# Kernel tuning notes

Hardware: AMD Instinct MI355X
Metric: run time of the kernel (lower is better)

## Reference

```python
import jax, jax.numpy as jnp
import numpy as np
from functools import partial

DN = ('NCHW', 'OIHW', 'NCHW')

def conv2d(x, w, b, stride):
    y = jax.lax.conv_general_dilated(x, w, (stride, stride), 'VALID', dimension_numbers=DN)
    return y + b[None, :, None, None]

def squash(s, eps=1e-8):
    norm = jnp.linalg.norm(s, axis=-1, keepdims=True)
    return (norm ** 2 / (1 + norm ** 2)) * s / (norm + eps)

def setup_inputs() -> dict:
    key = jax.random.key(0)
    ks = jax.random.split(key, 10)
    B, H, W = 16, 32, 512
    F, CAPS, E, OD = 64, 8, 8, 16
    H1 = (H - 6) // 2 + 1          # 14
    W1 = (W - 6) // 2 + 1          # 254
    N = F * H1 * W1 // CAPS        # 28448
    s = 0.05
    return {
        'x': jax.random.normal(ks[0], (B, H, W), jnp.float32),
        'conv1_w': jax.random.normal(ks[1], (F, 1, 6, 6), jnp.float32) * s,
        'conv1_b': jnp.zeros((F,), jnp.float32),
        'conv2_w': jax.random.normal(ks[2], (F, F, 6, 6), jnp.float32) * s,
        'conv2_b': jnp.zeros((F,), jnp.float32),
        'conv3_w': jax.random.normal(ks[3], (F, 2 * F, 1, 1), jnp.float32) * s,
        'conv3_b': jnp.zeros((F,), jnp.float32),
        'pc_w': jax.random.normal(ks[4], (N, CAPS, CAPS), jnp.float32) * s,  # [N, in, out]
        'pc_b': jnp.zeros((N, CAPS), jnp.float32),
        'ec_w': jax.random.normal(ks[5], (N, E, OD, CAPS), jnp.float32),
    }

def reference(x, conv1_w, conv1_b, conv2_w, conv2_b, conv3_w, conv3_b, pc_w, pc_b, ec_w):
    CAPS = pc_w.shape[1]
    NUM_ITER = 3
    B = x.shape[0]
    h = x[:, None]                                  # [B,1,H,W]
    h = jax.nn.relu(conv2d(h, conv1_w, conv1_b, 2)) # [B,F,14,254]
    y = jnp.pad(h, ((0, 0), (0, 0), (2, 3), (2, 3)))  # ZeroPad2d((2,3,2,3))
    y = jax.nn.relu(conv2d(y, conv2_w, conv2_b, 1))
    h = jax.nn.relu(jnp.concatenate((h, y), axis=1))
    h = conv2d(h, conv3_w, conv3_b, 1)              # [B,F,14,254]
    u_in = h.reshape(B, -1, CAPS)                   # [B,N,caps_len]
    # PrimaryCaps: N independent Linear(caps,caps) -> one batched einsum
    u = jnp.einsum('bni,nio->bno', u_in, pc_w) + pc_b[None]
    # EmotionCaps: per-capsule prediction u_hat [B,N,E,out_dim]
    u_hat = jnp.einsum('neoi,bni->bneo', ec_w, u)
    N, E = ec_w.shape[0], ec_w.shape[1]
    b_log = jnp.zeros((B, N, E), u_hat.dtype)
    v = None
    for r in range(NUM_ITER):
        c = jax.nn.softmax(b_log, axis=2)           # [B,N,E]
        s = jnp.einsum('bne,bneo->beo', c, u_hat)   # [B,E,out_dim]
        v = squash(s)
        if r < NUM_ITER - 1:
            b_log = b_log + jnp.einsum('bneo,beo->bne', u_hat, v)
    return jnp.linalg.norm(v, axis=-1)              # [B,E]
```

## Files before the change

kernel.cpp:

```cpp
#include <hip/hip_runtime.h>
#include <hip/hip_bf16.h>
#include <math.h>

#define BB 16
#define H1 14
#define W1 254
#define HPH 19
#define HPW2 264
#define NCAP 28448
#define FLATSZ 227584

typedef __attribute__((ext_vector_type(8))) short bf16x8;
typedef __attribute__((ext_vector_type(4))) float f32x4;
typedef __attribute__((ext_vector_type(2))) __fp16 f16x2;
typedef __attribute__((ext_vector_type(4))) uint uint4v;

__device__ __forceinline__ ushort f2bf(float f) {
  __hip_bfloat16 h = __float2bfloat16(f);
  return *(ushort*)&h;
}

__global__ __launch_bounds__(256) void prep_w(const float* __restrict__ w2, const float* __restrict__ w3,
                                              ushort* __restrict__ wb, float* __restrict__ w3t) {
  int idx = blockIdx.x * 256 + threadIdx.x;
  if (idx < 147456) {
    int co = idx / 2304; int rem = idx - co * 2304;
    int tap = rem >> 6; int ci = rem & 63;
    wb[idx] = f2bf(w2[(co * 64 + ci) * 36 + tap]);
  }
  if (idx < 8192) {
    int co = idx & 63; int c = idx >> 6;
    w3t[idx] = w3[co * 128 + c];
  }
}

__global__ __launch_bounds__(256) void cvt_ec(const float* __restrict__ ecw, uint* __restrict__ ech) {
  size_t i = (size_t)blockIdx.x * 256 + threadIdx.x;
  const float4* s = (const float4*)ecw + i * 2;
  float4 a = s[0], b = s[1];
  uint4v pk;
  { f16x2 h = __builtin_amdgcn_cvt_pkrtz(a.x, a.y); pk.x = *(uint*)&h; }
  { f16x2 h = __builtin_amdgcn_cvt_pkrtz(a.z, a.w); pk.y = *(uint*)&h; }
  { f16x2 h = __builtin_amdgcn_cvt_pkrtz(b.x, b.y); pk.z = *(uint*)&h; }
  { f16x2 h = __builtin_amdgcn_cvt_pkrtz(b.z, b.w); pk.w = *(uint*)&h; }
  *((uint4v*)ech + i) = pk;
}

__global__ __launch_bounds__(256) void conv1_k(const float* __restrict__ x, const float* __restrict__ w1,
                                               const float* __restrict__ b1, float* __restrict__ hc) {
  const int i = blockIdx.x, b = blockIdx.y;
  __shared__ float xs[6 * 512];
  __shared__ float wsh[2304];
  __shared__ float bsh[64];
  const int t = threadIdx.x;
  for (int idx = t; idx < 6 * 512; idx += 256) {
    int r = idx >> 9, c = idx & 511;
    xs[idx] = x[((size_t)b * 32 + 2 * i + r) * 512 + c];
  }
  for (int idx = t; idx < 2304; idx += 256) wsh[idx] = w1[idx];
  if (t < 64) bsh[t] = b1[t];
  __syncthreads();
  if (t < 254) {
    for (int c = 0; c < 64; c++) {
      float acc = bsh[c];
#pragma unroll
      for (int p = 0; p < 6; p++)
#pragma unroll
        for (int q = 0; q < 6; q++)
          acc = fmaf(xs[p * 512 + 2 * t + q], wsh[c * 36 + p * 6 + q], acc);
      acc = fmaxf(acc, 0.f);
      hc[(((size_t)b * 64 + c) * H1 + i) * W1 + t] = acc;
    }
  }
}

__global__ __launch_bounds__(256) void nhwc_k(const float* __restrict__ hc, ushort* __restrict__ hpc) {
  const int ct = blockIdx.x, i = blockIdx.y, b = blockIdx.z;
  const int c0 = ct * 64;
  __shared__ float ls[64 * 65];
  const int t = threadIdx.x;
  for (int idx = t; idx < 4096; idx += 256) {
    int ci = idx >> 6, cc = idx & 63;
    int c = c0 + cc;
    ls[ci * 65 + cc] = (c < W1) ? hc[(((size_t)b * 64 + ci) * H1 + i) * W1 + c] : 0.f;
  }
  __syncthreads();
  uint* outp = (uint*)hpc;
  for (int idx = t; idx < 2048; idx += 256) {
    int cc = idx >> 5, ci2 = idx & 31;
    int c = c0 + cc;
    if (c < W1) {
      float f0 = ls[(2 * ci2) * 65 + cc];
      float f1 = ls[(2 * ci2 + 1) * 65 + cc];
      uint pk = (uint)f2bf(f0) | ((uint)f2bf(f1) << 16);
      outp[(((size_t)b * HPH + 2 + i) * HPW2 + 2 + c) * 32 + ci2] = pk;
    }
  }
}

__device__ __forceinline__ void stage_b(const ushort* __restrict__ wb, ushort* __restrict__ bbuf,
                                        int tap, int w, int l) {
#pragma unroll
  for (int r = 0; r < 2; r++) {
    int v = r * 256 + w * 64 + l;
    int co = v >> 3, s = v & 7;
    int g = s ^ (co & 7);
    const ushort* gp = wb + co * 2304 + tap * 64 + g * 8;
    ushort* lp = bbuf + (size_t)(r * 256 + w * 64) * 8;
    __builtin_amdgcn_global_load_lds((const uint*)gp, (uint*)lp, 16, 0, 0);
  }
}

__global__ __launch_bounds__(256, 1) void conv2_mfma(const ushort* __restrict__ hpc,
                                                     const ushort* __restrict__ wb,
                                                     const float* __restrict__ b2, float* __restrict__ y) {
  const int b = blockIdx.z, i = blockIdx.y, j0 = blockIdx.x * 128;
  const int t = threadIdx.x;
  const int w = t >> 6, l = t & 63;
  const int lr = l & 15, quad = l >> 4;

  __shared__ ushort bls[2][4096];

  f32x4 acc[2][4];
#pragma unroll
  for (int mt = 0; mt < 2; mt++)
#pragma unroll
    for (int nt = 0; nt < 4; nt++) acc[mt][nt] = (f32x4){0.f, 0.f, 0.f, 0.f};

  const ushort* abase = hpc + (((size_t)b * HPH + i) * HPW2 + (j0 + w * 32 + lr)) * 64 + quad * 8;

  bf16x8 a0[2][2], a1[2][2];

#define ALOAD(dst, tap)                                                        \
  {                                                                            \
    const int p_ = (tap) / 6, q_ = (tap) % 6;                                  \
    const ushort* ap_ = abase + ((size_t)p_ * HPW2 + q_) * 64;                 \
    dst[0][0] = *(const bf16x8*)(ap_);                                         \
    dst[0][1] = *(const bf16x8*)(ap_ + 1024);                                  \
    dst[1][0] = *(const bf16x8*)(ap_ + 32);                                    \
    dst[1][1] = *(const bf16x8*)(ap_ + 32 + 1024);                             \
  }

#define COMPUTE(a, bp)                                                         \
  {                                                                            \
    _Pragma("unroll")                                                          \
    for (int ch = 0; ch < 2; ch++) {                                           \
      const int g2 = ch * 4 + quad;                                            \
      _Pragma("unroll")                                                        \
      for (int nt = 0; nt < 4; nt++) {                                         \
        const int co = nt * 16 + lr;                                           \
        bf16x8 bf = *(const bf16x8*)((bp) + co * 64 + ((g2 ^ (co & 7)) * 8));  \
        acc[0][nt] = __builtin_amdgcn_mfma_f32_16x16x32_bf16(a[ch][0], bf, acc[0][nt], 0, 0, 0); \
        acc[1][nt] = __builtin_amdgcn_mfma_f32_16x16x32_bf16(a[ch][1], bf, acc[1][nt], 0, 0, 0); \
      }                                                                        \
    }                                                                          \
  }

  stage_b(wb, &bls[0][0], 0, w, l);
  __syncthreads();
  ALOAD(a0, 0);

  for (int tp = 0; tp < 36; tp += 2) {
    stage_b(wb, &bls[1][0], tp + 1, w, l);
    ALOAD(a1, tp + 1);
    COMPUTE(a0, &bls[0][0]);
    __syncthreads();
    if (tp + 2 < 36) {
      stage_b(wb, &bls[0][0], tp + 2, w, l);
      ALOAD(a0, tp + 2);
    }
    COMPUTE(a1, &bls[1][0]);
    __syncthreads();
  }

#pragma unroll
  for (int nt = 0; nt < 4; nt++) {
    const int co = nt * 16 + lr;
    const float bias = b2[co];
    float* yrow = y + (((size_t)b * 64 + co) * H1 + i) * W1;
#pragma unroll
    for (int mt = 0; mt < 2; mt++) {
      const int jb = j0 + w * 32 + mt * 16 + quad * 4;
#pragma unroll
      for (int r = 0; r < 4; r++) {
        int j = jb + r;
        if (j < W1) yrow[j] = fmaxf(acc[mt][nt][r] + bias, 0.f);
      }
    }
  }
#undef ALOAD
#undef COMPUTE
}

__global__ __launch_bounds__(256) void conv3_k(const float* __restrict__ hc, const float* __restrict__ y,
                                               const float* __restrict__ w3t, const float* __restrict__ b3,
                                               float* __restrict__ out3) {
  const int b = blockIdx.z, i = blockIdx.y, j0 = blockIdx.x * 64;
  __shared__ float cs[32][64];
  __shared__ float wsh[32][64];
  const int t = threadIdx.x;
  const int cog = t >> 4, jg = t & 15;
  float acc[4][4];
#pragma unroll
  for (int a = 0; a < 4; a++)
#pragma unroll
    for (int j = 0; j < 4; j++) acc[a][j] = 0.f;

  for (int ch = 0; ch < 4; ch++) {
    __syncthreads();
    for (int idx = t; idx < 2048; idx += 256) {
      int cl = idx >> 6; int j = j0 + (idx & 63);
      int c = ch * 32 + cl;
      float v = 0.f;
      if (j < W1) {
        if (c < 64) v = hc[(((size_t)b * 64 + c) * H1 + i) * W1 + j];
        else        v = y[(((size_t)b * 64 + (c - 64)) * H1 + i) * W1 + j];
      }
      cs[cl][idx & 63] = v;
    }
    for (int idx = t; idx < 2048; idx += 256)
      wsh[idx >> 6][idx & 63] = w3t[(ch * 32 + (idx >> 6)) * 64 + (idx & 63)];
    __syncthreads();
#pragma unroll
    for (int c = 0; c < 32; c++) {
      float4 xv = *(const float4*)&cs[c][jg * 4];
      float4 wv = *(const float4*)&wsh[c][cog * 4];
#pragma unroll
      for (int jj = 0; jj < 4; jj++) {
        float xx = (&xv.x)[jj];
        acc[0][jj] = fmaf(wv.x, xx, acc[0][jj]);
        acc[1][jj] = fmaf(wv.y, xx, acc[1][jj]);
        acc[2][jj] = fmaf(wv.z, xx, acc[2][jj]);
        acc[3][jj] = fmaf(wv.w, xx, acc[3][jj]);
      }
    }
  }
#pragma unroll
  for (int a = 0; a < 4; a++) {
    int co = cog * 4 + a;
    float bias = b3[co];
#pragma unroll
    for (int jj = 0; jj < 4; jj++) {
      int j = j0 + jg * 4 + jj;
      if (j < W1) out3[(((size_t)b * 64 + co) * H1 + i) * W1 + j] = acc[a][jj] + bias;
    }
  }
}

__global__ __launch_bounds__(256) void pc_k(const float* __restrict__ out3, const float* __restrict__ pcw,
                                            const float* __restrict__ pcb, float* __restrict__ u) {
  int n = blockIdx.x * 256 + threadIdx.x;
  if (n >= NCAP) return;
  float pw[64];
  const float4* pwp = (const float4*)(pcw + (size_t)n * 64);
#pragma unroll
  for (int k = 0; k < 16; k++) {
    float4 v = pwp[k];
    pw[4 * k] = v.x; pw[4 * k + 1] = v.y; pw[4 * k + 2] = v.z; pw[4 * k + 3] = v.w;
  }
  float pb[8];
  {
    const float4* pbp = (const float4*)(pcb + (size_t)n * 8);
    float4 a = pbp[0], b = pbp[1];
    pb[0] = a.x; pb[1] = a.y; pb[2] = a.z; pb[3] = a.w;
    pb[4] = b.x; pb[5] = b.y; pb[6] = b.z; pb[7] = b.w;
  }
  for (int b = 0; b < BB; b++) {
    const float4* uip = (const float4*)(out3 + (size_t)b * FLATSZ + (size_t)n * 8);
    float4 a = uip[0], c = uip[1];
    float ui[8] = {a.x, a.y, a.z, a.w, c.x, c.y, c.z, c.w};
    float uo[8];
#pragma unroll
    for (int o = 0; o < 8; o++) uo[o] = pb[o];
#pragma unroll
    for (int i2 = 0; i2 < 8; i2++)
#pragma unroll
      for (int o = 0; o < 8; o++) uo[o] = fmaf(ui[i2], pw[i2 * 8 + o], uo[o]);
    float4* up = (float4*)(u + ((size_t)b * NCAP + n) * 8);
    up[0] = make_float4(uo[0], uo[1], uo[2], uo[3]);
    up[1] = make_float4(uo[4], uo[5], uo[6], uo[7]);
  }
}

template <int CTRL>
__device__ __forceinline__ float dpp_add(float x) {
  int y = __builtin_amdgcn_update_dpp(0, __float_as_int(x), CTRL, 0xF, 0xF, true);
  return x + __int_as_float(y);
}

template <int MODE>
__global__ __launch_bounds__(256, 4) void route5_k(const float* __restrict__ u, const uint* __restrict__ ech,
                                                   const float* __restrict__ v, float* __restrict__ sout) {
  __shared__ float red[4096];
  __shared__ float vlds[1024];
  float* us = red;

  const int t = threadIdx.x, l = t & 63, wv = t >> 6;
  const int b0 = blockIdx.y * 8;
  const int n0 = blockIdx.x * 32 + wv * 8;
  const int xaddr = (l ^ 32) << 2;

  if (MODE) {
    for (int idx = t; idx < 1024; idx += 256) vlds[idx] = v[b0 * 128 + idx];
  }
#pragma unroll
  for (int bb = 0; bb < 8; bb++)
    us[wv * 512 + bb * 64 + l] = u[((size_t)(b0 + bb) * NCAP + n0) * 8 + l];
  if (MODE) __syncthreads();

  float sacc[16];
#pragma unroll
  for (int k = 0; k < 16; k++) sacc[k] = 0.f;

  const uint4v* hbase = (const uint4v*)(ech + (size_t)n0 * 512) + (l * 2);

  auto proc = [&](int nn, uint4v w0, uint4v w1) {
    float ec[16];
#pragma unroll
    for (int k = 0; k < 4; k++) {
      uint t0 = w0[k], t1 = w1[k];
      f16x2 a = *(f16x2*)&t0;
      f16x2 b = *(f16x2*)&t1;
      ec[2 * k]     = (float)a.x; ec[2 * k + 1] = (float)a.y;
      ec[8 + 2 * k] = (float)b.x; ec[8 + 2 * k + 1] = (float)b.y;
    }
#pragma unroll
    for (int bb = 0; bb < 8; bb++) {
      const float4* up = (const float4*)&us[wv * 512 + bb * 64 + nn * 8];
      const float4 ua = up[0], ub = up[1];
      const float uv[8] = {ua.x, ua.y, ua.z, ua.w, ub.x, ub.y, ub.z, ub.w};
      float h0 = 0.f, h1 = 0.f;
#pragma unroll
      for (int k = 0; k < 8; k++) {
        h0 = fmaf(ec[k], uv[k], h0);
        h1 = fmaf(ec[8 + k], uv[k], h1);
      }
      if (MODE == 0) {
        sacc[2 * bb] += h0;
        sacc[2 * bb + 1] += h1;
      } else {
        const float2 vv = *(const float2*)&vlds[bb * 128 + 2 * l];
        float p = fmaf(h0, vv.x, h1 * vv.y);
        p = dpp_add<0xB1>(p);
        p = dpp_add<0x4E>(p);
        p = dpp_add<0x141>(p);
        const float ex = __expf(p);
        float den = dpp_add<0x140>(ex);
        den += __int_as_float(__builtin_amdgcn_ds_swizzle(__float_as_int(den), 0x401F));
        den += __int_as_float(__builtin_amdgcn_ds_bpermute(xaddr, __float_as_int(den)));
        const float cc = ex * __builtin_amdgcn_rcpf(den);
        sacc[2 * bb] = fmaf(cc, h0, sacc[2 * bb]);
        sacc[2 * bb + 1] = fmaf(cc, h1, sacc[2 * bb + 1]);
      }
    }
  };

  uint4v ca0 = hbase[0], ca1 = hbase[1];
#pragma unroll 1
  for (int nn = 0; nn < 8; nn += 2) {
    const uint4v* pb = hbase + (size_t)(nn + 1) * 128;
    uint4v cb0 = pb[0], cb1 = pb[1];
    proc(nn, ca0, ca1);
    if (nn + 2 < 8) {
      const uint4v* pa = hbase + (size_t)(nn + 2) * 128;
      ca0 = pa[0]; ca1 = pa[1];
    }
    proc(nn + 1, cb0, cb1);
  }

  __syncthreads();
#pragma unroll
  for (int k = 0; k < 16; k++) red[k * 256 + wv * 64 + l] = sacc[k];
  __syncthreads();
#pragma unroll
  for (int m = 0; m < 4; m++) {
    int slot = t + 256 * m;
    int bl = slot >> 7, eo = slot & 127;
    int k = 2 * bl + (eo & 1), l2 = eo >> 1;
    const float* r = red + k * 256 + l2;
    atomicAdd(&sout[(b0 + bl) * 128 + eo], r[0] + r[64] + r[128] + r[192]);
  }
}

__global__ void squash_k(const float* __restrict__ s, float scale, const float* __restrict__ vprev,
                         float* __restrict__ vout) {
  int t = threadIdx.x;
  const float* sp = s + t * 16;
  float sv[16]; float nn = 0.f;
#pragma unroll
  for (int o = 0; o < 16; o++) { float x = sp[o] * scale; sv[o] = x; nn = fmaf(x, x, nn); }
  float norm = sqrtf(nn);
  float f = nn / (1.f + nn) / (norm + 1e-8f);
#pragma unroll
  for (int o = 0; o < 16; o++) {
    float base = vprev ? vprev[t * 16 + o] : 0.f;
    vout[t * 16 + o] = base + f * sv[o];
  }
}

__global__ void squash_out_k(const float* __restrict__ s, float* __restrict__ out) {
  int t = threadIdx.x;
  float nn = 0.f;
#pragma unroll
  for (int o = 0; o < 16; o++) { float x = s[t * 16 + o]; nn = fmaf(x, x, nn); }
  float norm = sqrtf(nn);
  float f = nn / (1.f + nn) / (norm + 1e-8f);
  out[t] = f * norm;
}

extern "C" void kernel_launch(void* const* d_in, const int* in_sizes, int n_in,
                              void* d_out, int out_size, void* d_ws, size_t ws_size,
                              hipStream_t stream) {
  const float* x   = (const float*)d_in[0];
  const float* w1  = (const float*)d_in[1];
  const float* b1  = (const float*)d_in[2];
  const float* w2  = (const float*)d_in[3];
  const float* b2  = (const float*)d_in[4];
  const float* w3  = (const float*)d_in[5];
  const float* b3  = (const float*)d_in[6];
  const float* pcw = (const float*)d_in[7];
  const float* pcb = (const float*)d_in[8];
  const float* ecw = (const float*)d_in[9];
  float* out = (float*)d_out;

  float* ws = (float*)d_ws;
  size_t o = 0;
  float* hc   = ws + o; o += 3641344;
  float* yb   = ws + o; o += 3641344;
  float* out3 = ws + o; o += 3641344;
  ushort* hpc = (ushort*)(ws + o); o += 2568192;
  ushort* wb  = (ushort*)(ws + o); o += 73728;
  float* w3t  = ws + o; o += 8192;
  float* s0   = ws + o; o += 2048;
  float* s1   = ws + o; o += 2048;
  float* s2   = ws + o; o += 2048;
  float* v0   = ws + o; o += 2048;
  float* v1   = ws + o; o += 2048;
  uint* ech   = (uint*)(ws + o); o += 14565376;
  float* ub   = hc;

  hipMemsetAsync(hpc, 0, (size_t)16 * HPH * HPW2 * 64 * 2, stream);
  hipMemsetAsync(s0, 0, 3 * 2048 * 4, stream);

  prep_w<<<576, 256, 0, stream>>>(w2, w3, wb, w3t);
  cvt_ec<<<14224, 256, 0, stream>>>(ecw, ech);
  conv1_k<<<dim3(14, 16), 256, 0, stream>>>(x, w1, b1, hc);
  nhwc_k<<<dim3(4, 14, 16), 256, 0, stream>>>(hc, hpc);
  conv2_mfma<<<dim3(2, 14, 16), 256, 0, stream>>>(hpc, wb, b2, yb);
  conv3_k<<<dim3(4, 14, 16), 256, 0, stream>>>(hc, yb, w3t, b3, out3);
  pc_k<<<112, 256, 0, stream>>>(out3, pcw, pcb, ub);

  route5_k<0><<<dim3(889, 2), 256, 0, stream>>>(ub, ech, nullptr, s0);
  squash_k<<<1, 128, 0, stream>>>(s0, 0.125f, nullptr, v0);
  route5_k<1><<<dim3(889, 2), 256, 0, stream>>>(ub, ech, v0, s1);
  squash_k<<<1, 128, 0, stream>>>(s1, 1.0f, v0, v1);
  route5_k<1><<<dim3(889, 2), 256, 0, stream>>>(ub, ech, v1, s2);
  squash_out_k<<<1, 128, 0, stream>>>(s2, out);
}
```

Measured before the change: 478.1 us.

## Use f16 MFMA for capsule routing with fp16 u and all batches per block

Adds a kernel that converts the primary-capsule outputs u to fp16 in an [n][b][i] layout. The scalar-FMA routing kernel is replaced by one that computes u_hat with 16x16x32 f16 MFMA, covering all 16 batches per block, which halves the grid. The first pass sums four capsules per MFMA directly. The later passes run one capsule at a time, with a DPP row reduction for the agreement dot product and a per-row softmax over emotions. This moves the u·ec products onto matrix cores and stops reloading u for each batch half, at the cost of fp16 rounding of u and of the intermediate u_hat, plus MFMA lanes that sit idle in the routing passes.

```diff
diff --git a/kernel.cpp b/kernel.cpp
--- a/kernel.cpp
+++ b/kernel.cpp
@@ -13,11 +13,19 @@
 typedef __attribute__((ext_vector_type(8))) short bf16x8;
 typedef __attribute__((ext_vector_type(4))) float f32x4;
 typedef __attribute__((ext_vector_type(2))) __fp16 f16x2;
+typedef __attribute__((ext_vector_type(8))) _Float16 h8;
 typedef __attribute__((ext_vector_type(4))) uint uint4v;
 
 __device__ __forceinline__ ushort f2bf(float f) {
   __hip_bfloat16 h = __float2bfloat16(f);
   return *(ushort*)&h;
+}
+
+__device__ __forceinline__ h8 h8zero() {
+  h8 x;
+#pragma unroll
+  for (int z = 0; z < 8; z++) x[z] = (_Float16)0.f;
+  return x;
 }
 
 __global__ __launch_bounds__(256) void prep_w(const float* __restrict__ w2, const float* __restrict__ w3,
@@ -44,6 +52,17 @@
   { f16x2 h = __builtin_amdgcn_cvt_pkrtz(b.x, b.y); pk.z = *(uint*)&h; }
   { f16x2 h = __builtin_amdgcn_cvt_pkrtz(b.z, b.w); pk.w = *(uint*)&h; }
   *((uint4v*)ech + i) = pk;
+}
+
+__global__ __launch_bounds__(256) void cvt_u(const float* __restrict__ u, _Float16* __restrict__ uh) {
+  const int idx = blockIdx.x * 256 + threadIdx.x;
+  const int n = idx >> 4, b = idx & 15;
+  const float4* s = (const float4*)(u + ((size_t)b * NCAP + n) * 8);
+  float4 xa = s[0], xb = s[1];
+  h8 o;
+  o[0] = (_Float16)xa.x; o[1] = (_Float16)xa.y; o[2] = (_Float16)xa.z; o[3] = (_Float16)xa.w;
+  o[4] = (_Float16)xb.x; o[5] = (_Float16)xb.y; o[6] = (_Float16)xb.z; o[7] = (_Float16)xb.w;
+  *(h8*)(uh + (size_t)idx * 8) = o;
 }
 
 __global__ __launch_bounds__(256) void conv1_k(const float* __restrict__ x, const float* __restrict__ w1,
@@ -289,96 +308,90 @@
 }
 
 template <int MODE>
-__global__ __launch_bounds__(256, 4) void route5_k(const float* __restrict__ u, const uint* __restrict__ ech,
-                                                   const float* __restrict__ v, float* __restrict__ sout) {
-  __shared__ float red[4096];
-  __shared__ float vlds[1024];
-  float* us = red;
-
+__global__ __launch_bounds__(256, 4) void route6_k(const _Float16* __restrict__ uh,
+                                                   const _Float16* __restrict__ ech,
+                                                   const float* __restrict__ v,
+                                                   float* __restrict__ sout) {
+  __shared__ float red[8192];
+  __shared__ float vlds[2048];
   const int t = threadIdx.x, l = t & 63, wv = t >> 6;
-  const int b0 = blockIdx.y * 8;
+  const int q = l >> 4, lo = l & 15;
   const int n0 = blockIdx.x * 32 + wv * 8;
-  const int xaddr = (l ^ 32) << 2;
 
   if (MODE) {
-    for (int idx = t; idx < 1024; idx += 256) vlds[idx] = v[b0 * 128 + idx];
-  }
-#pragma unroll
-  for (int bb = 0; bb < 8; bb++)
-    us[wv * 512 + bb * 64 + l] = u[((size_t)(b0 + bb) * NCAP + n0) * 8 + l];
-  if (MODE) __syncthreads();
-
-  float sacc[16];
-#pragma unroll
-  for (int k = 0; k < 16; k++) sacc[k] = 0.f;
-
-  const uint4v* hbase = (const uint4v*)(ech + (size_t)n0 * 512) + (l * 2);
-
-  auto proc = [&](int nn, uint4v w0, uint4v w1) {
-    float ec[16];
-#pragma unroll
-    for (int k = 0; k < 4; k++) {
-      uint t0 = w0[k], t1 = w1[k];
-      f16x2 a = *(f16x2*)&t0;
-      f16x2 b = *(f16x2*)&t1;
-      ec[2 * k]     = (float)a.x; ec[2 * k + 1] = (float)a.y;
-      ec[8 + 2 * k] = (float)b.x; ec[8 + 2 * k + 1] = (float)b.y;
-    }
-#pragma unroll
-    for (int bb = 0; bb < 8; bb++) {
-      const float4* up = (const float4*)&us[wv * 512 + bb * 64 + nn * 8];
-      const float4 ua = up[0], ub = up[1];
-      const float uv[8] = {ua.x, ua.y, ua.z, ua.w, ub.x, ub.y, ub.z, ub.w};
-      float h0 = 0.f, h1 = 0.f;
-#pragma unroll
-      for (int k = 0; k < 8; k++) {
-        h0 = fmaf(ec[k], uv[k], h0);
-        h1 = fmaf(ec[8 + k], uv[k], h1);
-      }
-      if (MODE == 0) {
-        sacc[2 * bb] += h0;
-        sacc[2 * bb + 1] += h1;
-      } else {
-        const float2 vv = *(const float2*)&vlds[bb * 128 + 2 * l];
-        float p = fmaf(h0, vv.x, h1 * vv.y);
-        p = dpp_add<0xB1>(p);
-        p = dpp_add<0x4E>(p);
-        p = dpp_add<0x141>(p);
-        const float ex = __expf(p);
-        float den = dpp_add<0x140>(ex);
-        den += __int_as_float(__builtin_amdgcn_ds_swizzle(__float_as_int(den), 0x401F));
-        den += __int_as_float(__builtin_amdgcn_ds_bpermute(xaddr, __float_as_int(den)));
-        const float cc = ex * __builtin_amdgcn_rcpf(den);
-        sacc[2 * bb] = fmaf(cc, h0, sacc[2 * bb]);
-        sacc[2 * bb + 1] = fmaf(cc, h1, sacc[2 * bb + 1]);
-      }
-    }
-  };
-
-  uint4v ca0 = hbase[0], ca1 = hbase[1];
+    for (int idx = t; idx < 2048; idx += 256) vlds[idx] = v[idx];
+    __syncthreads();
+  }
+
+  f32x4 sacc[8];
+#pragma unroll
+  for (int e = 0; e < 8; e++) sacc[e] = (f32x4){0.f, 0.f, 0.f, 0.f};
+
+  if (MODE == 0) {
 #pragma unroll 1
-  for (int nn = 0; nn < 8; nn += 2) {
-    const uint4v* pb = hbase + (size_t)(nn + 1) * 128;
-    uint4v cb0 = pb[0], cb1 = pb[1];
-    proc(nn, ca0, ca1);
-    if (nn + 2 < 8) {
-      const uint4v* pa = hbase + (size_t)(nn + 2) * 128;
-      ca0 = pa[0]; ca1 = pa[1];
-    }
-    proc(nn + 1, cb0, cb1);
-  }
-
+    for (int g = 0; g < 2; g++) {
+      const int nb = n0 + g * 4;
+      h8 a = *(const h8*)(uh + ((size_t)(nb + q) * 16 + lo) * 8);
+#pragma unroll
+      for (int e = 0; e < 8; e++) {
+        h8 b = *(const h8*)(ech + (((size_t)(nb + q) * 8 + e) * 16 + lo) * 8);
+        sacc[e] = __builtin_amdgcn_mfma_f32_16x16x32_f16(a, b, sacc[e], 0, 0, 0);
+      }
+    }
+  } else {
+    const float* vbase = vlds + q * 512 + lo;
+#pragma unroll 1
+    for (int nn = 0; nn < 8; nn++) {
+      const int n = n0 + nn;
+      h8 a = h8zero();
+      if (l < 16) a = *(const h8*)(uh + ((size_t)n * 16 + lo) * 8);
+      uint cpk[8][2];
+      float ex[4][8];
+      float den[4] = {0.f, 0.f, 0.f, 0.f};
+#pragma unroll
+      for (int e = 0; e < 8; e++) {
+        h8 b = h8zero();
+        if (l < 16) b = *(const h8*)(ech + (((size_t)n * 8 + e) * 16 + lo) * 8);
+        f32x4 c = __builtin_amdgcn_mfma_f32_16x16x32_f16(a, b, (f32x4){0.f, 0.f, 0.f, 0.f}, 0, 0, 0);
+        { f16x2 hh = __builtin_amdgcn_cvt_pkrtz(c[0], c[1]); cpk[e][0] = *(uint*)&hh; }
+        { f16x2 hh = __builtin_amdgcn_cvt_pkrtz(c[2], c[3]); cpk[e][1] = *(uint*)&hh; }
+#pragma unroll
+        for (int r = 0; r < 4; r++) {
+          float pr = c[r] * vbase[r * 128 + e * 16];
+          pr = dpp_add<0xB1>(pr);
+          pr = dpp_add<0x4E>(pr);
+          pr = dpp_add<0x141>(pr);
+          pr = dpp_add<0x140>(pr);
+          float exx = __expf(pr);
+          ex[r][e] = exx;
+          den[r] += exx;
+        }
+      }
+      float rd[4];
+#pragma unroll
+      for (int r = 0; r < 4; r++) rd[r] = __builtin_amdgcn_rcpf(den[r]);
+#pragma unroll
+      for (int e = 0; e < 8; e++) {
+        f16x2 u0 = *(f16x2*)&cpk[e][0];
+        f16x2 u1 = *(f16x2*)&cpk[e][1];
+        sacc[e][0] = fmaf(ex[0][e] * rd[0], (float)u0.x, sacc[e][0]);
+        sacc[e][1] = fmaf(ex[1][e] * rd[1], (float)u0.y, sacc[e][1]);
+        sacc[e][2] = fmaf(ex[2][e] * rd[2], (float)u1.x, sacc[e][2]);
+        sacc[e][3] = fmaf(ex[3][e] * rd[3], (float)u1.y, sacc[e][3]);
+      }
+    }
+  }
+
+#pragma unroll
+  for (int e = 0; e < 8; e++)
+#pragma unroll
+    for (int r = 0; r < 4; r++)
+      red[wv * 2048 + (4 * q + r) * 128 + e * 16 + lo] = sacc[e][r];
   __syncthreads();
 #pragma unroll
-  for (int k = 0; k < 16; k++) red[k * 256 + wv * 64 + l] = sacc[k];
-  __syncthreads();
-#pragma unroll
-  for (int m = 0; m < 4; m++) {
-    int slot = t + 256 * m;
-    int bl = slot >> 7, eo = slot & 127;
-    int k = 2 * bl + (eo & 1), l2 = eo >> 1;
-    const float* r = red + k * 256 + l2;
-    atomicAdd(&sout[(b0 + bl) * 128 + eo], r[0] + r[64] + r[128] + r[192]);
+  for (int m = 0; m < 8; m++) {
+    const int slot = t + 256 * m;
+    atomicAdd(&sout[slot], red[slot] + red[2048 + slot] + red[4096 + slot] + red[6144 + slot]);
   }
 }
 
@@ -438,6 +451,7 @@
   float* v1   = ws + o; o += 2048;
   uint* ech   = (uint*)(ws + o); o += 14565376;
   float* ub   = hc;
+  _Float16* uhp = (_Float16*)yb;
 
   hipMemsetAsync(hpc, 0, (size_t)16 * HPH * HPW2 * 64 * 2, stream);
   hipMemsetAsync(s0, 0, 3 * 2048 * 4, stream);
@@ -449,11 +463,13 @@
   conv2_mfma<<<dim3(2, 14, 16), 256, 0, stream>>>(hpc, wb, b2, yb);
   conv3_k<<<dim3(4, 14, 16), 256, 0, stream>>>(hc, yb, w3t, b3, out3);
   pc_k<<<112, 256, 0, stream>>>(out3, pcw, pcb, ub);
-
-  route5_k<0><<<dim3(889, 2), 256, 0, stream>>>(ub, ech, nullptr, s0);
+  cvt_u<<<1778, 256, 0, stream>>>(ub, uhp);
+
+  const _Float16* echh = (const _Float16*)ech;
+  route6_k<0><<<889, 256, 0, stream>>>(uhp, echh, nullptr, s0);
   squash_k<<<1, 128, 0, stream>>>(s0, 0.125f, nullptr, v0);
-  route5_k<1><<<dim3(889, 2), 256, 0, stream>>>(ub, ech, v0, s1);
+  route6_k<1><<<889, 256, 0, stream>>>(uhp, echh, v0, s1);
   squash_k<<<1, 128, 0, stream>>>(s1, 1.0f, v0, v1);
-  route5_k<1><<<dim3(889, 2), 256, 0, stream>>>(ub, ech, v1, s2);
+  route6_k<1><<<889, 256, 0, stream>>>(uhp, echh, v1, s2);
   squash_out_k<<<1, 128, 0, stream>>>(s2, out);
 }
```

After: 584.3 us. +22.2%, slower.

## Use MFMA f16 for first routing pass and permlane32 swap for reductions

Applied to the files above, without the earlier changes.

Adds a kernel that converts u to fp16 in an n-major, batch-interleaved layout. The first routing iteration, which is a plain sum over capsules, now runs as MFMA 16x16x32 f16 products over all 16 batches in one block, replacing the scalar FMA path. The later iterations drop the LDS staging of v and load it into registers, and they swap the bpermute xor-32 exchange for permlane32_swap where that builtin exists. The added conversion pass costs extra memory traffic, and fp16 u lowers precision in the first pass.

```diff
diff --git a/kernel.cpp b/kernel.cpp
--- a/kernel.cpp
+++ b/kernel.cpp
@@ -13,6 +13,7 @@
 typedef __attribute__((ext_vector_type(8))) short bf16x8;
 typedef __attribute__((ext_vector_type(4))) float f32x4;
 typedef __attribute__((ext_vector_type(2))) __fp16 f16x2;
+typedef __attribute__((ext_vector_type(8))) _Float16 h8;
 typedef __attribute__((ext_vector_type(4))) uint uint4v;
 
 __device__ __forceinline__ ushort f2bf(float f) {
@@ -44,6 +45,17 @@
   { f16x2 h = __builtin_amdgcn_cvt_pkrtz(b.x, b.y); pk.z = *(uint*)&h; }
   { f16x2 h = __builtin_amdgcn_cvt_pkrtz(b.z, b.w); pk.w = *(uint*)&h; }
   *((uint4v*)ech + i) = pk;
+}
+
+__global__ __launch_bounds__(256) void cvt_u(const float* __restrict__ u, _Float16* __restrict__ uh) {
+  const int idx = blockIdx.x * 256 + threadIdx.x;
+  const int n = idx >> 4, b = idx & 15;
+  const float4* s = (const float4*)(u + ((size_t)b * NCAP + n) * 8);
+  float4 xa = s[0], xb = s[1];
+  h8 o;
+  o[0] = (_Float16)xa.x; o[1] = (_Float16)xa.y; o[2] = (_Float16)xa.z; o[3] = (_Float16)xa.w;
+  o[4] = (_Float16)xb.x; o[5] = (_Float16)xb.y; o[6] = (_Float16)xb.z; o[7] = (_Float16)xb.w;
+  *(h8*)(uh + (size_t)idx * 8) = o;
 }
 
 __global__ __launch_bounds__(256) void conv1_k(const float* __restrict__ x, const float* __restrict__ w1,
@@ -288,25 +300,70 @@
   return x + __int_as_float(y);
 }
 
-template <int MODE>
-__global__ __launch_bounds__(256, 4) void route5_k(const float* __restrict__ u, const uint* __restrict__ ech,
+__device__ __forceinline__ float xor32_partner(float x, bool low) {
+#if __has_builtin(__builtin_amdgcn_permlane32_swap)
+  auto r = __builtin_amdgcn_permlane32_swap(__float_as_uint(x), __float_as_uint(x), false, false);
+  return __uint_as_float(low ? r[1] : r[0]);
+#else
+  return __uint_as_float((uint)__builtin_amdgcn_ds_bpermute(
+      (int)((((threadIdx.x & 63) ^ 32) << 2)), (int)__float_as_uint(x)));
+#endif
+}
+
+__global__ __launch_bounds__(256, 4) void route_s0(const _Float16* __restrict__ uh,
+                                                   const _Float16* __restrict__ ech,
+                                                   float* __restrict__ sout) {
+  __shared__ float red[8192];
+  const int t = threadIdx.x, l = t & 63, wv = t >> 6;
+  const int q = l >> 4, lo = l & 15;
+  const int n0 = blockIdx.x * 32 + wv * 8;
+
+  f32x4 sacc[8];
+#pragma unroll
+  for (int e = 0; e < 8; e++) sacc[e] = (f32x4){0.f, 0.f, 0.f, 0.f};
+
+#pragma unroll 1
+  for (int g = 0; g < 2; g++) {
+    const int nb = n0 + g * 4;
+    h8 a = *(const h8*)(uh + ((size_t)(nb + q) * 16 + lo) * 8);
+#pragma unroll
+    for (int e = 0; e < 8; e++) {
+      h8 b = *(const h8*)(ech + (((size_t)(nb + q) * 8 + e) * 16 + lo) * 8);
+      sacc[e] = __builtin_amdgcn_mfma_f32_16x16x32_f16(a, b, sacc[e], 0, 0, 0);
+    }
+  }
+
+#pragma unroll
+  for (int e = 0; e < 8; e++)
+#pragma unroll
+    for (int r = 0; r < 4; r++)
+      red[wv * 2048 + (4 * q + r) * 128 + e * 16 + lo] = sacc[e][r];
+  __syncthreads();
+#pragma unroll
+  for (int m = 0; m < 8; m++) {
+    const int slot = t + 256 * m;
+    atomicAdd(&sout[slot], red[slot] + red[2048 + slot] + red[4096 + slot] + red[6144 + slot]);
+  }
+}
+
+__global__ __launch_bounds__(256, 4) void route_s1(const float* __restrict__ u, const uint* __restrict__ ech,
                                                    const float* __restrict__ v, float* __restrict__ sout) {
   __shared__ float red[4096];
-  __shared__ float vlds[1024];
   float* us = red;
 
   const int t = threadIdx.x, l = t & 63, wv = t >> 6;
   const int b0 = blockIdx.y * 8;
   const int n0 = blockIdx.x * 32 + wv * 8;
-  const int xaddr = (l ^ 32) << 2;
-
-  if (MODE) {
-    for (int idx = t; idx < 1024; idx += 256) vlds[idx] = v[b0 * 128 + idx];
-  }
+  const bool low = l < 32;
+
+  float2 vv[8];
+#pragma unroll
+  for (int bb = 0; bb < 8; bb++)
+    vv[bb] = *(const float2*)&v[(size_t)(b0 + bb) * 128 + 2 * l];
+
 #pragma unroll
   for (int bb = 0; bb < 8; bb++)
     us[wv * 512 + bb * 64 + l] = u[((size_t)(b0 + bb) * NCAP + n0) * 8 + l];
-  if (MODE) __syncthreads();
 
   float sacc[16];
 #pragma unroll
@@ -335,23 +392,17 @@
         h0 = fmaf(ec[k], uv[k], h0);
         h1 = fmaf(ec[8 + k], uv[k], h1);
       }
-      if (MODE == 0) {
-        sacc[2 * bb] += h0;
-        sacc[2 * bb + 1] += h1;
-      } else {
-        const float2 vv = *(const float2*)&vlds[bb * 128 + 2 * l];
-        float p = fmaf(h0, vv.x, h1 * vv.y);
-        p = dpp_add<0xB1>(p);
-        p = dpp_add<0x4E>(p);
-        p = dpp_add<0x141>(p);
-        const float ex = __expf(p);
-        float den = dpp_add<0x140>(ex);
-        den += __int_as_float(__builtin_amdgcn_ds_swizzle(__float_as_int(den), 0x401F));
-        den += __int_as_float(__builtin_amdgcn_ds_bpermute(xaddr, __float_as_int(den)));
-        const float cc = ex * __builtin_amdgcn_rcpf(den);
-        sacc[2 * bb] = fmaf(cc, h0, sacc[2 * bb]);
-        sacc[2 * bb + 1] = fmaf(cc, h1, sacc[2 * bb + 1]);
-      }
+      float p = fmaf(h0, vv[bb].x, h1 * vv[bb].y);
+      p = dpp_add<0xB1>(p);
+      p = dpp_add<0x4E>(p);
+      p = dpp_add<0x141>(p);
+      const float ex = __expf(p);
+      float den = dpp_add<0x140>(ex);
+      den += __int_as_float(__builtin_amdgcn_ds_swizzle(__float_as_int(den), 0x401F));
+      den += xor32_partner(den, low);
+      const float cc = ex * __builtin_amdgcn_rcpf(den);
+      sacc[2 * bb] = fmaf(cc, h0, sacc[2 * bb]);
+      sacc[2 * bb + 1] = fmaf(cc, h1, sacc[2 * bb + 1]);
     }
   };
 
@@ -438,6 +489,7 @@
   float* v1   = ws + o; o += 2048;
   uint* ech   = (uint*)(ws + o); o += 14565376;
   float* ub   = hc;
+  _Float16* uhp = (_Float16*)yb;
 
   hipMemsetAsync(hpc, 0, (size_t)16 * HPH * HPW2 * 64 * 2, stream);
   hipMemsetAsync(s0, 0, 3 * 2048 * 4, stream);
@@ -449,11 +501,12 @@
   conv2_mfma<<<dim3(2, 14, 16), 256, 0, stream>>>(hpc, wb, b2, yb);
   conv3_k<<<dim3(4, 14, 16), 256, 0, stream>>>(hc, yb, w3t, b3, out3);
   pc_k<<<112, 256, 0, stream>>>(out3, pcw, pcb, ub);
-
-  route5_k<0><<<dim3(889, 2), 256, 0, stream>>>(ub, ech, nullptr, s0);
+  cvt_u<<<1778, 256, 0, stream>>>(ub, uhp);
+
+  route_s0<<<889, 256, 0, stream>>>(uhp, (const _Float16*)ech, s0);
   squash_k<<<1, 128, 0, stream>>>(s0, 0.125f, nullptr, v0);
-  route5_k<1><<<dim3(889, 2), 256, 0, stream>>>(ub, ech, v0, s1);
+  route_s1<<<dim3(889, 2), 256, 0, stream>>>(ub, ech, v0, s1);
   squash_k<<<1, 128, 0, stream>>>(s1, 1.0f, v0, v1);
-  route5_k<1><<<dim3(889, 2), 256, 0, stream>>>(ub, ech, v1, s2);
+  route_s1<<<dim3(889, 2), 256, 0, stream>>>(ub, ech, v1, s2);
   squash_out_k<<<1, 128, 0, stream>>>(s2, out);
 }
```

Result: no change. 472.6 us (-1.1%).
